# Performance work log

Measured on AMD Instinct MI355X. Metric: run time of the kernel, lower is better.

Reference implementation:

```python
import jax, jax.numpy as jnp
import numpy as np

N_NODES = 50000
N_EDGES = 800000
D = 256          # in_features == out_features == num_classes
T = 4            # number of replicas / linear heads
NS = 64          # num_edges (hyperedges)


def setup_inputs() -> dict:
    key = jax.random.key(0)
    ks = jax.random.split(key, 10)
    s = D ** -0.5
    return {
        "edge_index": jax.random.randint(ks[0], (2, N_EDGES), 0, N_NODES, dtype=jnp.int64)
        if jax.config.jax_enable_x64 else jax.random.randint(ks[0], (2, N_EDGES), 0, N_NODES, dtype=jnp.int32),
        "features": jax.random.normal(ks[1], (N_NODES, D), jnp.float32),
        "lin_w": jax.random.normal(ks[2], (T, D, D), jnp.float32) * s,
        "lin_b": jax.random.normal(ks[3], (T, D), jnp.float32) * 0.01,
        "gcn0_w": jax.random.normal(ks[4], (D, D), jnp.float32) * s,
        "gcn0_b": jax.random.normal(ks[5], (D,), jnp.float32) * 0.01,
        "gcn1_w": jax.random.normal(ks[6], (D, D), jnp.float32) * s,
        "gcn1_b": jax.random.normal(ks[7], (D,), jnp.float32) * 0.01,
        "lin1_w": jax.random.normal(ks[8], (D, NS), jnp.float32) * s,
        "lin1_b": jax.random.normal(ks[9], (NS,), jnp.float32) * 0.01,
    }


def _l2_normalize(x, eps=1e-8):
    n = jnp.sqrt(jnp.sum(x * x, axis=-1, keepdims=True))
    return x / jnp.maximum(n, eps)


def reference(edge_index, features, lin_w, lin_b, gcn0_w, gcn0_b, gcn1_w, gcn1_b, lin1_w, lin1_b):
    num_nodes, d = features.shape
    t = lin_w.shape[0]
    ns = lin1_w.shape[1]
    scale = d ** -0.5  # out_features ** -0.5

    # t linear projections: (t, N, D)
    transformed = jnp.einsum('nd,tdk->tnk', features, lin_w) + lin_b[:, None, :]

    src, dst = edge_index[0], edge_index[1]
    # cosine similarity of features[src] vs each replica's transformed[dst]
    fs = _l2_normalize(features)[src]              # (E, D)
    tf_n = _l2_normalize(transformed)              # (t, N, D)
    sim = jnp.stack([jnp.sum(fs * tf_n[i][dst], axis=-1) for i in range(t)], axis=1)  # (E, t)
    best_idx = jnp.argmax(sim, axis=1)
    best_dst = dst + best_idx.astype(dst.dtype) * num_nodes

    # extra per-replica identity edges: node n -> node n + i*N, i in [0, t)
    ar = jnp.arange(num_nodes, dtype=src.dtype)
    extra_src = jnp.tile(ar, t)
    extra_dst = (ar[None, :] + (jnp.arange(t, dtype=src.dtype) * num_nodes)[:, None]).reshape(-1)

    src_all = jnp.concatenate([src, src, extra_src])
    dst_all = jnp.concatenate([dst, best_dst, extra_dst])
    n_total = (t + 1) * num_nodes

    # PyG gcn_norm: drop pre-existing self loops (weight 0), add one self loop per node,
    # symmetric normalization with degree from destination index.
    loops = jnp.arange(n_total, dtype=src.dtype)
    src2 = jnp.concatenate([src_all, loops])
    dst2 = jnp.concatenate([dst_all, loops])
    w2 = jnp.concatenate([jnp.where(src_all == dst_all, 0.0, 1.0).astype(features.dtype),
                          jnp.ones(n_total, features.dtype)])
    deg = jax.ops.segment_sum(w2, dst2, num_segments=n_total)
    dinv = jnp.where(deg > 0, jax.lax.rsqrt(deg), 0.0)
    norm = w2 * dinv[src2] * dinv[dst2]

    def gcn(x, W, b):
        xw = x @ W
        return jax.ops.segment_sum(norm[:, None] * xw[src2], dst2, num_segments=n_total) + b

    all_features = jnp.concatenate([features, transformed.reshape(t * num_nodes, d)], axis=0)
    # dropout is identity in eval mode
    h = jax.nn.relu(all_features)
    h = gcn(h, gcn0_w, gcn0_b)
    h = jax.nn.relu(h)
    all_features2 = gcn(h, gcn1_w, gcn1_b)          # ((t+1)N, D)
    logits = jax.nn.relu(all_features2) @ lin1_w + lin1_b  # ((t+1)N, NS)

    # H[n, c] counts how many of the (t+1) replicas assign node n to cluster c
    classes = jnp.argmax(logits.reshape(t + 1, num_nodes, ns), axis=-1)  # (t+1, N)
    H = jax.nn.one_hot(classes, ns, dtype=features.dtype).sum(axis=0)     # (N, NS)

    # hyperedge features: sum of all_features2 over base-replica nodes in each hyperedge
    mask = (H > 0).astype(features.dtype)                                  # (N, NS)
    hyperedge_features = mask.T @ all_features2[:num_nodes]                # (NS, D)

    dots = (all_features @ hyperedge_features.T) * scale                   # ((t+1)N, NS)
    return H, hyperedge_features, dots
```

## Files before the change

### kernel.cpp

```cpp
#include <hip/hip_runtime.h>

#define D 256
#define T 4
#define NS 64

typedef unsigned int uint32;
typedef short s16x8 __attribute__((ext_vector_type(8)));
typedef float f32x4 __attribute__((ext_vector_type(4)));

__device__ __forceinline__ float bflo(uint32 u) { return __uint_as_float(u << 16); }
__device__ __forceinline__ float bfhi(uint32 u) { return __uint_as_float(u & 0xffff0000u); }
__device__ __forceinline__ unsigned short f2bf(float x) {
    uint32 u = __float_as_uint(x);
    u = u + 0x7FFFu + ((u >> 16) & 1u);
    return (unsigned short)(u >> 16);
}
__device__ __forceinline__ uint32 pack2(float a, float b) {
    return (uint32)f2bf(a) | ((uint32)f2bf(b) << 16);
}
__device__ __forceinline__ uint32 relu2(uint32 u) {
    uint32 s = u & 0x80008000u;
    uint32 m = ((s >> 15) ^ 0x00010001u) * 0xFFFFu;
    return u & m;
}

__global__ void zero_kernel(uint32* __restrict__ p, long long n)
{
    long long i = (long long)blockIdx.x * blockDim.x + threadIdx.x;
    long long st = (long long)gridDim.x * blockDim.x;
    for (; i < n; i += st) p[i] = 0u;
}

__global__ void f2bf_kernel(const float* __restrict__ in, unsigned short* __restrict__ out,
                            long long n8)
{
    long long i = (long long)blockIdx.x * blockDim.x + threadIdx.x;
    long long st = (long long)gridDim.x * blockDim.x;
    for (; i < n8; i += st) {
        float4 a = *(const float4*)(in + i * 8);
        float4 b = *(const float4*)(in + i * 8 + 4);
        uint4 o;
        o.x = pack2(a.x, a.y); o.y = pack2(a.z, a.w);
        o.z = pack2(b.x, b.y); o.w = pack2(b.z, b.w);
        *(uint4*)(out + i * 8) = o;
    }
}

__global__ void wfrag_kernel(const float* __restrict__ g0, const float* __restrict__ g1,
                             const float* __restrict__ lw, unsigned short* __restrict__ out)
{
    int o = blockIdx.x * 256 + threadIdx.x;
    int mat = blockIdx.y;
    const float* W = (mat == 0) ? g0 : (mat == 1) ? g1 : (lw + (size_t)(mat - 2) * 65536);
    int j = o & 7, lane = (o >> 3) & 63, ks = (o >> 9) & 7, nt = o >> 12;
    int n15 = lane & 15, quad = lane >> 4;
    int k = ks * 32 + quad * 8 + j;
    int n = nt * 16 + n15;
    out[(size_t)mat * 65536 + o] = f2bf(W[(size_t)k * 256 + n]);
}

__global__ __launch_bounds__(256, 2)
void gemm_mfma(const unsigned short* __restrict__ A,
               const unsigned short* __restrict__ Wfrag,
               const float* __restrict__ bias,
               unsigned short* __restrict__ Cout,
               int M, int nStripes)
{
    __shared__ unsigned short Asm[64 * 264];
    int t = threadIdx.x, w = t >> 6, lane = t & 63;
    int n15 = lane & 15, quad = lane >> 4;
    int z = blockIdx.y;
    Wfrag += (size_t)z * 65536;
    bias  += (size_t)z * 256;
    Cout  += (size_t)z * (size_t)M * 256;

    s16x8 bfr[4][8];
#pragma unroll
    for (int nt = 0; nt < 4; nt++)
#pragma unroll
        for (int ks = 0; ks < 8; ks++)
            bfr[nt][ks] = *(const s16x8*)(Wfrag +
                (size_t)(((w * 4 + nt) * 8 + ks) * 64 + lane) * 8);

    float bcol[4];
#pragma unroll
    for (int nt = 0; nt < 4; nt++) bcol[nt] = bias[(w * 4 + nt) * 16 + n15];

    for (int s = blockIdx.x; s < nStripes; s += gridDim.x) {
        int m0 = s * 64;
        __syncthreads();
#pragma unroll
        for (int i = 0; i < 8; i++) {
            int idx = i * 256 + t;
            int m = idx >> 5, kc = (idx & 31) * 8;
            int gm = m0 + m;
            uint4 v = make_uint4(0u, 0u, 0u, 0u);
            if (gm < M) v = *(const uint4*)(A + (size_t)gm * 256 + kc);
            *(uint4*)(Asm + m * 264 + kc) = v;
        }
        __syncthreads();

        f32x4 acc[4][4];
#pragma unroll
        for (int rt = 0; rt < 4; rt++)
#pragma unroll
            for (int nt = 0; nt < 4; nt++)
#pragma unroll
                for (int e = 0; e < 4; e++) acc[rt][nt][e] = 0.f;

#pragma unroll
        for (int rt = 0; rt < 4; rt++) {
            int abase = (rt * 16 + n15) * 264 + quad * 8;
#pragma unroll
            for (int ks = 0; ks < 8; ks++) {
                s16x8 a = *(const s16x8*)(Asm + abase + ks * 32);
#pragma unroll
                for (int nt = 0; nt < 4; nt++)
                    acc[rt][nt] = __builtin_amdgcn_mfma_f32_16x16x32_bf16(
                        a, bfr[nt][ks], acc[rt][nt], 0, 0, 0);
            }
        }

#pragma unroll
        for (int rt = 0; rt < 4; rt++) {
            int row0 = m0 + rt * 16 + quad * 4;
#pragma unroll
            for (int nt = 0; nt < 4; nt++) {
                int colp = (w * 4 + nt) * 16 + n15;
#pragma unroll
                for (int r = 0; r < 4; r++) {
                    int gr = row0 + r;
                    if (gr < M)
                        Cout[(size_t)gr * 256 + colp] = f2bf(acc[rt][nt][r] + bcol[nt]);
                }
            }
        }
    }
}

__global__ __launch_bounds__(256)
void tinv_kernel(const unsigned short* __restrict__ tr, float* __restrict__ tinv, int rows)
{
    int wave = threadIdx.x >> 6, lane = threadIdx.x & 63;
    int r = blockIdx.x * 4 + wave;
    if (r >= rows) return;
    uint2 q = *(const uint2*)(tr + (size_t)r * D + lane * 4);
    float a = bflo(q.x), b = bfhi(q.x), c = bflo(q.y), d = bfhi(q.y);
    float s = a * a + b * b + c * c + d * d;
#pragma unroll
    for (int off = 32; off; off >>= 1) s += __shfl_xor(s, off);
    if (lane == 0) tinv[r] = 1.f / fmaxf(sqrtf(s), 1e-8f);
}

__global__ void ehist_kernel(const int* __restrict__ dst, int* __restrict__ ecnt, int E)
{
    for (int e = blockIdx.x * blockDim.x + threadIdx.x; e < E;
         e += gridDim.x * blockDim.x)
        atomicAdd(ecnt + dst[e], 1);
}

__global__ void escatter_kernel(const int* __restrict__ src, const int* __restrict__ dst,
                                const int* __restrict__ eptr, int* __restrict__ efill,
                                uint2* __restrict__ esorted, int E)
{
    for (int e = blockIdx.x * blockDim.x + threadIdx.x; e < E;
         e += gridDim.x * blockDim.x) {
        int d = dst[e];
        int pos = eptr[d] + atomicAdd(efill + d, 1);
        esorted[pos] = make_uint2((uint32)src[e], (uint32)d);
    }
}

__global__ __launch_bounds__(256)
void sim3_kernel(const uint2* __restrict__ esorted,
                 const unsigned short* __restrict__ featb,
                 const unsigned short* __restrict__ tr, const float* __restrict__ tinv,
                 int* __restrict__ bestS, int E, int Nn)
{
    int w = threadIdx.x >> 6, lane = threadIdx.x & 63;
    int n15 = lane & 15, quad = lane >> 4;
    int base = (blockIdx.x * 4 + w) * 16;
    if (base >= E) return;
    int ei = min(base + n15, E - 1);
    uint2 se = esorted[ei];
    const unsigned short* arow = featb + (size_t)se.x * D + quad * 8;
    const unsigned short* brow = tr + (size_t)se.y * D + quad * 8;
    size_t rstride = (size_t)Nn * D;

    f32x4 a0 = {0.f, 0.f, 0.f, 0.f}, a1 = a0, a2 = a0, a3 = a0;
#pragma unroll
    for (int ks = 0; ks < 8; ks++) {
        s16x8 a  = *(const s16x8*)(arow + ks * 32);
        s16x8 b0 = *(const s16x8*)(brow + ks * 32);
        s16x8 b1 = *(const s16x8*)(brow + rstride + ks * 32);
        s16x8 b2 = *(const s16x8*)(brow + 2 * rstride + ks * 32);
        s16x8 b3 = *(const s16x8*)(brow + 3 * rstride + ks * 32);
        a0 = __builtin_amdgcn_mfma_f32_16x16x32_bf16(a, b0, a0, 0, 0, 0);
        a1 = __builtin_amdgcn_mfma_f32_16x16x32_bf16(a, b1, a1, 0, 0, 0);
        a2 = __builtin_amdgcn_mfma_f32_16x16x32_bf16(a, b2, a2, 0, 0, 0);
        a3 = __builtin_amdgcn_mfma_f32_16x16x32_bf16(a, b3, a3, 0, 0, 0);
    }
    if (quad == (n15 >> 2) && base + n15 < E) {
        int r = n15 & 3;
        int d = (int)se.y;
        float v0 = a0[r] * tinv[d];
        float v1 = a1[r] * tinv[Nn + d];
        float v2 = a2[r] * tinv[2 * Nn + d];
        float v3 = a3[r] * tinv[3 * Nn + d];
        float bv = v0; int bi = 0;
        if (v1 > bv) { bv = v1; bi = 1; }
        if (v2 > bv) { bv = v2; bi = 2; }
        if (v3 > bv) { bv = v3; bi = 3; }
        bestS[base + n15] = bi;
    }
}

__device__ __forceinline__ void decode_edge(int e, const uint2* __restrict__ esorted,
                                            const int* __restrict__ bestS,
                                            int E, int Nn, int& s, int& d, bool& keep)
{
    if (e < E) {
        uint2 se = esorted[e];
        s = (int)se.x; d = (int)se.y; keep = (s != d);
    } else if (e < 2 * E) {
        int k = e - E;
        uint2 se = esorted[k];
        s = (int)se.x; d = (int)se.y + bestS[k] * Nn; keep = (s != d);
    } else if (e < 2 * E + T * Nn) {
        int k = e - 2 * E; int i = k / Nn; int n = k - i * Nn;
        s = n; d = n + i * Nn; keep = (i != 0);
    } else {
        int v = e - (2 * E + T * Nn); s = v; d = v; keep = true;
    }
}

__global__ void hist_kernel(const uint2* __restrict__ esorted, const int* __restrict__ bestS,
                            int* __restrict__ cnt, int E, int Nn)
{
    int total = 2 * E + (2 * T + 1) * Nn;
    for (int e = blockIdx.x * blockDim.x + threadIdx.x; e < total;
         e += gridDim.x * blockDim.x) {
        int s, d; bool keep;
        decode_edge(e, esorted, bestS, E, Nn, s, d, keep);
        if (keep) atomicAdd(cnt + d, 1);
    }
}

__global__ void dinv_kernel(const int* __restrict__ cnt, float* __restrict__ dinv, int n)
{
    int v = blockIdx.x * blockDim.x + threadIdx.x;
    if (v < n) dinv[v] = (cnt[v] > 0) ? rsqrtf((float)cnt[v]) : 0.f;
}

__global__ void emeta_kernel(const uint2* __restrict__ esorted, const int* __restrict__ bestS,
                             const float* __restrict__ dinv, uint2* __restrict__ emeta, int E)
{
    for (int e = blockIdx.x * blockDim.x + threadIdx.x; e < E;
         e += gridDim.x * blockDim.x) {
        uint2 se = esorted[e];
        uint32 packed = se.x | ((uint32)bestS[e] << 27);
        emeta[e] = make_uint2(packed, __float_as_uint(dinv[se.x]));
    }
}

__global__ void scan_sums(const int* __restrict__ cnt, int* __restrict__ aux, int n)
{
    __shared__ int sd[256];
    int idx = blockIdx.x * 256 + threadIdx.x;
    sd[threadIdx.x] = (idx < n) ? cnt[idx] : 0;
    __syncthreads();
    for (int off = 128; off; off >>= 1) {
        if (threadIdx.x < off) sd[threadIdx.x] += sd[threadIdx.x + off];
        __syncthreads();
    }
    if (threadIdx.x == 0) aux[blockIdx.x] = sd[0];
}

__global__ void scan_aux(const int* __restrict__ aux, int* __restrict__ auxex, int nb)
{
    __shared__ int sd[1024];
    int t = threadIdx.x;
    int v = (t < nb) ? aux[t] : 0;
    sd[t] = v;
    __syncthreads();
    for (int off = 1; off < 1024; off <<= 1) {
        int x = (t >= off) ? sd[t - off] : 0;
        __syncthreads();
        sd[t] += x;
        __syncthreads();
    }
    if (t < nb) auxex[t] = sd[t] - v;
}

__global__ void scan_write(const int* __restrict__ cnt, const int* __restrict__ auxex,
                           int* __restrict__ rowptr, int n)
{
    __shared__ int sd[256];
    int t = threadIdx.x;
    int idx = blockIdx.x * 256 + t;
    int v = (idx < n) ? cnt[idx] : 0;
    sd[t] = v;
    __syncthreads();
    for (int off = 1; off < 256; off <<= 1) {
        int x = (t >= off) ? sd[t - off] : 0;
        __syncthreads();
        sd[t] += x;
        __syncthreads();
    }
    if (idx < n) {
        int rp = auxex[blockIdx.x] + sd[t] - v;
        rowptr[idx] = rp;
        if (idx == n - 1) rowptr[n] = rp + v;
    }
}

__global__ __launch_bounds__(256)
void agg5_kernel(const int* __restrict__ eptr, const uint2* __restrict__ emeta,
                 const unsigned short* __restrict__ xa,
                 const unsigned short* __restrict__ xb,
                 const float* __restrict__ dinv,
                 unsigned short* __restrict__ outb, int Nn)
{
    int wave = threadIdx.x >> 6, lane = threadIdx.x & 63;
    int v = blockIdx.x * 4 + wave;
    if (v >= Nn) return;

    float dv  = dinv[v];
    float dr1 = dinv[v + Nn];
    float dr2 = dinv[v + 2 * Nn];
    float dr3 = dinv[v + 3 * Nn];
    float dr4 = dinv[v + 4 * Nn];

    uint2 qv = *(const uint2*)(xa + (size_t)v * D + lane * 4);
    qv.x = relu2(qv.x); qv.y = relu2(qv.y);
    float y0 = bflo(qv.x), y1 = bfhi(qv.x), y2 = bflo(qv.y), y3 = bfhi(qv.y);

    float wsb = dv * dv;
    float b0 = wsb * y0, b1 = wsb * y1, b2 = wsb * y2, b3 = wsb * y3;

    float wi1 = dv * dr1, wi2 = dv * dr2, wi3 = dv * dr3;
    float r10 = wi1 * y0, r11 = wi1 * y1, r12 = wi1 * y2, r13 = wi1 * y3;
    float r20 = wi2 * y0, r21 = wi2 * y1, r22 = wi2 * y2, r23 = wi2 * y3;
    float r30 = wi3 * y0, r31 = wi3 * y1, r32 = wi3 * y2, r33 = wi3 * y3;
    float r40 = 0.f, r41 = 0.f, r42 = 0.f, r43 = 0.f;

    {
        uint2 q = *(const uint2*)(xb + ((size_t)0 * Nn + v) * D + lane * 4);
        q.x = relu2(q.x); q.y = relu2(q.y);
        float ws = dr1 * dr1;
        r10 = fmaf(ws, bflo(q.x), r10); r11 = fmaf(ws, bfhi(q.x), r11);
        r12 = fmaf(ws, bflo(q.y), r12); r13 = fmaf(ws, bfhi(q.y), r13);
    }
    {
        uint2 q = *(const uint2*)(xb + ((size_t)1 * Nn + v) * D + lane * 4);
        q.x = relu2(q.x); q.y = relu2(q.y);
        float ws = dr2 * dr2;
        r20 = fmaf(ws, bflo(q.x), r20); r21 = fmaf(ws, bfhi(q.x), r21);
        r22 = fmaf(ws, bflo(q.y), r22); r23 = fmaf(ws, bfhi(q.y), r23);
    }
    {
        uint2 q = *(const uint2*)(xb + ((size_t)2 * Nn + v) * D + lane * 4);
        q.x = relu2(q.x); q.y = relu2(q.y);
        float ws = dr3 * dr3;
        r30 = fmaf(ws, bflo(q.x), r30); r31 = fmaf(ws, bfhi(q.x), r31);
        r32 = fmaf(ws, bflo(q.y), r32); r33 = fmaf(ws, bfhi(q.y), r33);
    }
    {
        uint2 q = *(const uint2*)(xb + ((size_t)3 * Nn + v) * D + lane * 4);
        q.x = relu2(q.x); q.y = relu2(q.y);
        float ws = dr4 * dr4;
        r40 = fmaf(ws, bflo(q.x), r40); r41 = fmaf(ws, bfhi(q.x), r41);
        r42 = fmaf(ws, bflo(q.y), r42); r43 = fmaf(ws, bfhi(q.y), r43);
    }

    int j = eptr[v], jend = eptr[v + 1];

#define EDGE_BODY(qq, ss, bb, ww)                                                  \
    {                                                                              \
        float x0 = bflo(qq.x), x1 = bfhi(qq.x), x2 = bflo(qq.y), x3 = bfhi(qq.y);  \
        float wb = (ss != v) ? (ww) * dv : 0.f;                                    \
        if (bb == 0) wb += wb;                                                     \
        b0 = fmaf(wb, x0, b0); b1 = fmaf(wb, x1, b1);                              \
        b2 = fmaf(wb, x2, b2); b3 = fmaf(wb, x3, b3);                              \
        if (bb == 1) {                                                             \
            float wr = (ww) * dr1;                                                 \
            r10 = fmaf(wr, x0, r10); r11 = fmaf(wr, x1, r11);                      \
            r12 = fmaf(wr, x2, r12); r13 = fmaf(wr, x3, r13);                      \
        } else if (bb == 2) {                                                      \
            float wr = (ww) * dr2;                                                 \
            r20 = fmaf(wr, x0, r20); r21 = fmaf(wr, x1, r21);                      \
            r22 = fmaf(wr, x2, r22); r23 = fmaf(wr, x3, r23);                      \
        } else if (bb == 3) {                                                      \
            float wr = (ww) * dr3;                                                 \
            r30 = fmaf(wr, x0, r30); r31 = fmaf(wr, x1, r31);                      \
            r32 = fmaf(wr, x2, r32); r33 = fmaf(wr, x3, r33);                      \
        }                                                                          \
    }

    for (; j + 2 <= jend; j += 2) {
        uint2 m0 = emeta[j];
        uint2 m1 = emeta[j + 1];
        uint32 su0 = (uint32)__builtin_amdgcn_readfirstlane((int)m0.x);
        uint32 su1 = (uint32)__builtin_amdgcn_readfirstlane((int)m1.x);
        float ws0 = __uint_as_float((uint32)__builtin_amdgcn_readfirstlane((int)m0.y));
        float ws1 = __uint_as_float((uint32)__builtin_amdgcn_readfirstlane((int)m1.y));
        int s0 = (int)(su0 & 0x07FFFFFFu), bx0 = (int)(su0 >> 27);
        int s1 = (int)(su1 & 0x07FFFFFFu), bx1 = (int)(su1 >> 27);
        uint2 q0 = *(const uint2*)(xa + (size_t)s0 * D + lane * 4);
        uint2 q1 = *(const uint2*)(xa + (size_t)s1 * D + lane * 4);
        q0.x = relu2(q0.x); q0.y = relu2(q0.y);
        q1.x = relu2(q1.x); q1.y = relu2(q1.y);
        EDGE_BODY(q0, s0, bx0, ws0);
        EDGE_BODY(q1, s1, bx1, ws1);
    }
    if (j < jend) {
        uint2 m0 = emeta[j];
        uint32 su0 = (uint32)__builtin_amdgcn_readfirstlane((int)m0.x);
        float ws0 = __uint_as_float((uint32)__builtin_amdgcn_readfirstlane((int)m0.y));
        int s0 = (int)(su0 & 0x07FFFFFFu), bx0 = (int)(su0 >> 27);
        uint2 q0 = *(const uint2*)(xa + (size_t)s0 * D + lane * 4);
        q0.x = relu2(q0.x); q0.y = relu2(q0.y);
        EDGE_BODY(q0, s0, bx0, ws0);
    }
#undef EDGE_BODY

    uint2 o;
    o.x = pack2(b0, b1); o.y = pack2(b2, b3);
    *(uint2*)(outb + (size_t)v * D + lane * 4) = o;
    o.x = pack2(r10, r11); o.y = pack2(r12, r13);
    *(uint2*)(outb + ((size_t)v + Nn) * D + lane * 4) = o;
    o.x = pack2(r20, r21); o.y = pack2(r22, r23);
    *(uint2*)(outb + ((size_t)v + 2 * (size_t)Nn) * D + lane * 4) = o;
    o.x = pack2(r30, r31); o.y = pack2(r32, r33);
    *(uint2*)(outb + ((size_t)v + 3 * (size_t)Nn) * D + lane * 4) = o;
    o.x = pack2(r40, r41); o.y = pack2(r42, r43);
    *(uint2*)(outb + ((size_t)v + 4 * (size_t)Nn) * D + lane * 4) = o;
}

__global__ __launch_bounds__(256, 2)
void logits_mfma(const unsigned short* __restrict__ af2, const float* __restrict__ Wl,
                 const float* __restrict__ bl, float* __restrict__ H,
                 int M, int Nn, int nStripes)
{
    __shared__ unsigned short Asm[64 * 264];
    int t = threadIdx.x, w = t >> 6, lane = t & 63;
    int n15 = lane & 15, quad = lane >> 4;

    s16x8 bfr[4][8];
#pragma unroll
    for (int nt = 0; nt < 4; nt++)
#pragma unroll
        for (int ks = 0; ks < 8; ks++) {
            s16x8 f;
#pragma unroll
            for (int j = 0; j < 8; j++) {
                int k = ks * 32 + quad * 8 + j;
                f[j] = (short)f2bf(Wl[(size_t)k * NS + nt * 16 + n15]);
            }
            bfr[nt][ks] = f;
        }
    float bcol[4];
#pragma unroll
    for (int nt = 0; nt < 4; nt++) bcol[nt] = bl[nt * 16 + n15];

    for (int s = blockIdx.x; s < nStripes; s += gridDim.x) {
        int m0 = s * 64;
        __syncthreads();
#pragma unroll
        for (int i = 0; i < 8; i++) {
            int idx = i * 256 + t;
            int m = idx >> 5, kc = (idx & 31) * 8;
            int gm = m0 + m;
            uint4 v = make_uint4(0u, 0u, 0u, 0u);
            if (gm < M) {
                v = *(const uint4*)(af2 + (size_t)gm * 256 + kc);
                v.x = relu2(v.x); v.y = relu2(v.y);
                v.z = relu2(v.z); v.w = relu2(v.w);
            }
            *(uint4*)(Asm + m * 264 + kc) = v;
        }
        __syncthreads();

        f32x4 acc[4];
#pragma unroll
        for (int nt = 0; nt < 4; nt++)
#pragma unroll
            for (int e = 0; e < 4; e++) acc[nt][e] = 0.f;

        int abase = (w * 16 + n15) * 264 + quad * 8;
#pragma unroll
        for (int ks = 0; ks < 8; ks++) {
            s16x8 a = *(const s16x8*)(Asm + abase + ks * 32);
#pragma unroll
            for (int nt = 0; nt < 4; nt++)
                acc[nt] = __builtin_amdgcn_mfma_f32_16x16x32_bf16(
                    a, bfr[nt][ks], acc[nt], 0, 0, 0);
        }

#pragma unroll
        for (int e = 0; e < 4; e++) {
            float bv = acc[0][e] + bcol[0]; int bi = n15;
#pragma unroll
            for (int nt = 1; nt < 4; nt++) {
                float v = acc[nt][e] + bcol[nt];
                int c = nt * 16 + n15;
                if (v > bv) { bv = v; bi = c; }
            }
#pragma unroll
            for (int off = 1; off < 16; off <<= 1) {
                float ov = __shfl_xor(bv, off);
                int   oi = __shfl_xor(bi, off);
                if (ov > bv || (ov == bv && oi < bi)) { bv = ov; bi = oi; }
            }
            if (n15 == 0) {
                int gr = m0 + w * 16 + quad * 4 + e;
                if (gr < M) atomicAdd(H + (size_t)(gr % Nn) * NS + bi, 1.0f);
            }
        }
    }
}

__global__ __launch_bounds__(256)
void maskTb_kernel(const float* __restrict__ H, unsigned short* __restrict__ maskTb,
                   int Nn, int Kpad)
{
    __shared__ unsigned short tile[64 * 72];
    int t = threadIdx.x;
    int n0 = blockIdx.x * 64;
    int c = t & 63, rr = t >> 6;
#pragma unroll
    for (int i = 0; i < 16; i++) {
        int n = rr + i * 4;
        float hv = (n0 + n < Nn) ? H[(size_t)(n0 + n) * NS + c] : 0.f;
        tile[c * 72 + n] = (hv > 0.f) ? (unsigned short)0x3F80 : (unsigned short)0;
    }
    __syncthreads();
#pragma unroll
    for (int i = 0; i < 4; i++) {
        int idx = i * 256 + t;
        int cc = idx >> 4, ch = idx & 15;
        if (idx < 512) {
            cc = idx >> 3; ch = idx & 7;
            uint4 v = *(const uint4*)(tile + cc * 72 + ch * 8);
            *(uint4*)(maskTb + (size_t)cc * Kpad + n0 + ch * 8) = v;
        }
    }
}

__global__ __launch_bounds__(256, 2)
void he_gemm(const unsigned short* __restrict__ maskTb,
             const unsigned short* __restrict__ af2,
             float* __restrict__ partials, int Kpad)
{
    __shared__ unsigned short Bsm[32 * 264];
    int t = threadIdx.x, w = t >> 6, lane = t & 63;
    int n15 = lane & 15, quad = lane >> 4;
    int k0 = blockIdx.x * 256;

    f32x4 acc[4][4];
#pragma unroll
    for (int mt = 0; mt < 4; mt++)
#pragma unroll
        for (int nt = 0; nt < 4; nt++)
#pragma unroll
            for (int e = 0; e < 4; e++) acc[mt][nt][e] = 0.f;

    for (int s = 0; s < 8; s++) {
        int k = k0 + s * 32;
        __syncthreads();
#pragma unroll
        for (int i = 0; i < 4; i++) {
            int idx = i * 256 + t;
            int row = idx >> 5, col8 = (idx & 31) * 8;
            uint4 v = *(const uint4*)(af2 + (size_t)(k + row) * 256 + col8);
            *(uint4*)(Bsm + row * 264 + col8) = v;
        }
        __syncthreads();

        s16x8 a[4];
#pragma unroll
        for (int mt = 0; mt < 4; mt++)
            a[mt] = *(const s16x8*)(maskTb + (size_t)(mt * 16 + n15) * Kpad
                                    + k + quad * 8);
#pragma unroll
        for (int nt = 0; nt < 4; nt++) {
            int ncol = w * 64 + nt * 16 + n15;
            s16x8 b;
#pragma unroll
            for (int j = 0; j < 8; j++)
                b[j] = (short)Bsm[(quad * 8 + j) * 264 + ncol];
#pragma unroll
            for (int mt = 0; mt < 4; mt++)
                acc[mt][nt] = __builtin_amdgcn_mfma_f32_16x16x32_bf16(
                    a[mt], b, acc[mt][nt], 0, 0, 0);
        }
    }

    float* pdst = partials + (size_t)blockIdx.x * (64 * 256);
#pragma unroll
    for (int mt = 0; mt < 4; mt++)
#pragma unroll
        for (int nt = 0; nt < 4; nt++)
#pragma unroll
            for (int r = 0; r < 4; r++) {
                int m = mt * 16 + quad * 4 + r;
                int n = w * 64 + nt * 16 + n15;
                pdst[(size_t)m * 256 + n] = acc[mt][nt][r];
            }
}

__global__ __launch_bounds__(256)
void he_reduce2(const float* __restrict__ partials, float* __restrict__ he, int KB)
{
    int idx = blockIdx.x * 256 + threadIdx.x;
    float s = 0.f;
    for (int b = 0; b < KB; b++)
        s += partials[(size_t)b * 16384 + idx];
    he[idx] = s;
}

__global__ void bigb_copy(const float* __restrict__ he, float* __restrict__ BigB)
{
    int idx = blockIdx.x * 256 + threadIdx.x;
    if (idx < D * NS) {
        int d = idx >> 6, c = idx & 63;
        BigB[idx] = he[(size_t)c * D + d];
    }
}

__global__ __launch_bounds__(256)
void bigb_mm(const float* __restrict__ lin_w, const float* __restrict__ lin_b,
             const float* __restrict__ he, float* __restrict__ BigB,
             float* __restrict__ beta)
{
    int gw = (int)((blockIdx.x * 256 + threadIdx.x) >> 6);
    int lane = threadIdx.x & 63;
    const int totalA = T * D * NS;
    if (gw >= totalA + T * NS) return;
    const float* xrow; const float* hrow; float* outp;
    if (gw < totalA) {
        int t = gw / (D * NS); int rem = gw - t * D * NS;
        int d = rem / NS; int c = rem - d * NS;
        xrow = lin_w + ((size_t)t * D + d) * D;
        hrow = he + (size_t)c * D;
        outp = BigB + ((size_t)(t + 1) * D + d) * NS + c;
    } else {
        int i = gw - totalA; int t = i / NS; int c = i - t * NS;
        xrow = lin_b + (size_t)t * D;
        hrow = he + (size_t)c * D;
        outp = beta + (size_t)(t + 1) * NS + c;
    }
    float4 x = *(const float4*)(xrow + lane * 4);
    float4 h = *(const float4*)(hrow + lane * 4);
    float s = x.x * h.x + x.y * h.y + x.z * h.z + x.w * h.w;
#pragma unroll
    for (int off = 32; off; off >>= 1) s += __shfl_xor(s, off);
    if (lane == 0) *outp = s;
}

__global__ __launch_bounds__(256, 2)
void dots_mfma(const unsigned short* __restrict__ featb,
               const float* __restrict__ feat32, int useBf,
               const float* __restrict__ BigB,
               const float* __restrict__ beta, float* __restrict__ dots,
               int Nn, int nStripes)
{
    __shared__ unsigned short Asm[64 * 264];
    int t = threadIdx.x, w = t >> 6, lane = t & 63;
    int n15 = lane & 15, quad = lane >> 4;
    int rho = blockIdx.y;
    const float* Bp = BigB + (size_t)rho * D * NS;

    s16x8 bfr[4][8];
#pragma unroll
    for (int nt = 0; nt < 4; nt++)
#pragma unroll
        for (int ks = 0; ks < 8; ks++) {
            s16x8 f;
#pragma unroll
            for (int j = 0; j < 8; j++) {
                int k = ks * 32 + quad * 8 + j;
                f[j] = (short)f2bf(Bp[(size_t)k * NS + nt * 16 + n15]);
            }
            bfr[nt][ks] = f;
        }
    float bcol[4];
#pragma unroll
    for (int nt = 0; nt < 4; nt++) bcol[nt] = beta[rho * NS + nt * 16 + n15];

    for (int s = blockIdx.x; s < nStripes; s += gridDim.x) {
        int m0 = s * 64;
        __syncthreads();
#pragma unroll
        for (int i = 0; i < 8; i++) {
            int idx = i * 256 + t;
            int m = idx >> 5, kc = (idx & 31) * 8;
            int gm = m0 + m;
            uint4 o = make_uint4(0u, 0u, 0u, 0u);
            if (gm < Nn) {
                if (useBf) {
                    o = *(const uint4*)(featb + (size_t)gm * 256 + kc);
                } else {
                    float4 a = *(const float4*)(feat32 + (size_t)gm * 256 + kc);
                    float4 b = *(const float4*)(feat32 + (size_t)gm * 256 + kc + 4);
                    o.x = pack2(a.x, a.y); o.y = pack2(a.z, a.w);
                    o.z = pack2(b.x, b.y); o.w = pack2(b.z, b.w);
                }
            }
            *(uint4*)(Asm + m * 264 + kc) = o;
        }
        __syncthreads();

        f32x4 acc[4];
#pragma unroll
        for (int nt = 0; nt < 4; nt++)
#pragma unroll
            for (int e = 0; e < 4; e++) acc[nt][e] = 0.f;

        int abase = (w * 16 + n15) * 264 + quad * 8;
#pragma unroll
        for (int ks = 0; ks < 8; ks++) {
            s16x8 a = *(const s16x8*)(Asm + abase + ks * 32);
#pragma unroll
            for (int nt = 0; nt < 4; nt++)
                acc[nt] = __builtin_amdgcn_mfma_f32_16x16x32_bf16(
                    a, bfr[nt][ks], acc[nt], 0, 0, 0);
        }

#pragma unroll
        for (int e = 0; e < 4; e++) {
            int gr = m0 + w * 16 + quad * 4 + e;
            if (gr >= Nn) continue;
#pragma unroll
            for (int nt = 0; nt < 4; nt++) {
                int c = nt * 16 + n15;
                dots[((size_t)rho * Nn + gr) * NS + c] = (acc[nt][e] + bcol[nt]) * 0.0625f;
            }
        }
    }
}

extern "C" void kernel_launch(void* const* d_in, const int* in_sizes, int n_in,
                              void* d_out, int out_size, void* d_ws, size_t ws_size,
                              hipStream_t stream)
{
    const int*   edge_index = (const int*)d_in[0];
    const float* features   = (const float*)d_in[1];
    const float* lin_w      = (const float*)d_in[2];
    const float* lin_b      = (const float*)d_in[3];
    const float* gcn0_w     = (const float*)d_in[4];
    const float* gcn0_b     = (const float*)d_in[5];
    const float* gcn1_w     = (const float*)d_in[6];
    const float* gcn1_b     = (const float*)d_in[7];
    const float* lin1_w     = (const float*)d_in[8];
    const float* lin1_b     = (const float*)d_in[9];

    int E  = in_sizes[0] / 2;
    int Nn = in_sizes[1] / D;
    int n_total = (T + 1) * Nn;
    int Mrep = T * Nn;

    const int* src = edge_index;
    const int* dst = edge_index + E;

    float* out_H    = (float*)d_out;
    float* out_he   = out_H + (size_t)Nn * NS;
    float* out_dots = out_he + (size_t)NS * D;

    int KB   = (Nn + 255) / 256;
    int Kpad = KB * 256;

    char* ws0 = (char*)d_ws;
    char* wsp = ws0;
    auto carve = [&](size_t bytes) {
        char* p = wsp; wsp += (bytes + 255) & ~(size_t)255; return p;
    };
    unsigned short* R1   = (unsigned short*)carve((size_t)n_total * D * 2);
    unsigned short* R2   = (unsigned short*)carve((size_t)n_total * D * 2);
    float*          BigB = (float*)carve((size_t)(T + 1) * D * NS * 4);
    float*          beta = (float*)carve((size_t)(T + 1) * NS * 4);
    unsigned short* transformed = R2;

    size_t featb_bytes = (size_t)Nn * D * 2;
    unsigned short* featb = nullptr;
    int useBfDots = 0;
    if ((size_t)(wsp - ws0) + featb_bytes + 256 <= ws_size) {
        featb = (unsigned short*)carve(featb_bytes);
        useBfDots = 1;
    }

    char* sc = (char*)out_dots;
    auto carve2 = [&](size_t bytes) {
        char* p = sc; sc += (bytes + 255) & ~(size_t)255; return p;
    };
    float* tinv    = (float*)carve2((size_t)Mrep * 4);
    int*   best    = (int*)carve2((size_t)E * 4);
    int*   cnt     = (int*)carve2((size_t)n_total * 4);
    float* dinv    = (float*)carve2((size_t)n_total * 4);
    int*   aux     = (int*)carve2(1024 * 4);
    int*   auxex   = (int*)carve2(1024 * 4);
    if (!featb) featb = (unsigned short*)carve2(featb_bytes);
    unsigned short* Wfrags = (unsigned short*)carve2((size_t)6 * 65536 * 2);
    int*   ecnt    = (int*)carve2((size_t)Nn * 4);
    int*   eptr    = (int*)carve2((size_t)(Nn + 1) * 4);
    int*   efill   = (int*)carve2((size_t)Nn * 4);
    uint2* esorted = (uint2*)carve2((size_t)E * 8);
    uint2* emeta   = (uint2*)carve2((size_t)E * 8);
    unsigned short* maskTb = (unsigned short*)carve2((size_t)NS * Kpad * 2);

    float* partials = (float*)R1;

    zero_kernel<<<512, 256, 0, stream>>>((uint32*)cnt, n_total);
    zero_kernel<<<512, 256, 0, stream>>>((uint32*)ecnt, Nn);
    zero_kernel<<<512, 256, 0, stream>>>((uint32*)efill, Nn);
    zero_kernel<<<512, 256, 0, stream>>>((uint32*)out_H, (long long)Nn * NS + NS * D);
    zero_kernel<<<1, 256, 0, stream>>>((uint32*)beta, (T + 1) * NS);

    wfrag_kernel<<<dim3(256, 6), 256, 0, stream>>>(gcn0_w, gcn1_w, lin_w, Wfrags);
    f2bf_kernel<<<2048, 256, 0, stream>>>(features, featb, (long long)Nn * D / 8);

    int strN = (Nn + 63) / 64;
    gemm_mfma<<<dim3(512, T), 256, 0, stream>>>(featb, Wfrags + 2 * 65536, lin_b,
                                                transformed, Nn, strN);
    tinv_kernel<<<(Mrep + 3) / 4, 256, 0, stream>>>(transformed, tinv, Mrep);

    ehist_kernel<<<2048, 256, 0, stream>>>(dst, ecnt, E);
    int enb = (Nn + 255) / 256;
    scan_sums<<<enb, 256, 0, stream>>>(ecnt, aux, Nn);
    scan_aux<<<1, 1024, 0, stream>>>(aux, auxex, enb);
    scan_write<<<enb, 256, 0, stream>>>(ecnt, auxex, eptr, Nn);
    escatter_kernel<<<2048, 256, 0, stream>>>(src, dst, eptr, efill, esorted, E);
    int nGroups = (E + 15) / 16;
    sim3_kernel<<<(nGroups + 3) / 4, 256, 0, stream>>>(esorted, featb, transformed,
                                                       tinv, best, E, Nn);

    hist_kernel<<<2048, 256, 0, stream>>>(esorted, best, cnt, E, Nn);
    dinv_kernel<<<(n_total + 255) / 256, 256, 0, stream>>>(cnt, dinv, n_total);
    emeta_kernel<<<2048, 256, 0, stream>>>(esorted, best, dinv, emeta, E);

    int strT = (n_total + 63) / 64;
    agg5_kernel<<<(Nn + 3) / 4, 256, 0, stream>>>(eptr, emeta, featb, transformed,
                                                  dinv, R1, Nn);
    gemm_mfma<<<dim3(512, 1), 256, 0, stream>>>(R1, Wfrags, gcn0_b, R1, n_total, strT);

    agg5_kernel<<<(Nn + 3) / 4, 256, 0, stream>>>(eptr, emeta, R1, R1 + (size_t)Nn * D,
                                                  dinv, R2, Nn);
    gemm_mfma<<<dim3(512, 1), 256, 0, stream>>>(R2, Wfrags + 65536, gcn1_b, R2,
                                                n_total, strT);

    logits_mfma<<<512, 256, 0, stream>>>(R2, lin1_w, lin1_b, out_H, n_total, Nn, strT);

    maskTb_kernel<<<Kpad / 64, 256, 0, stream>>>(out_H, maskTb, Nn, Kpad);
    he_gemm<<<KB, 256, 0, stream>>>(maskTb, R2, partials, Kpad);
    he_reduce2<<<64, 256, 0, stream>>>(partials, out_he, KB);

    bigb_copy<<<(D * NS + 255) / 256, 256, 0, stream>>>(out_he, BigB);
    bigb_mm<<<(T * D * NS + T * NS + 3) / 4, 256, 0, stream>>>(lin_w, lin_b, out_he,
                                                               BigB, beta);
    dots_mfma<<<dim3(160, 5), 256, 0, stream>>>(featb, features, useBfDots,
                                                BigB, beta, out_dots, Nn, strN);
}
```

Before: 1.005 ms.

## Interleave replica outputs per node so similarity gathers read contiguous rows

The transformed projections are now stored node-major with the four replica rows adjacent (row = node*4 + replica), rather than replica-major. The edge-similarity kernel then reads all four replica rows for a destination node from one contiguous 2KB region, and it loads the source feature fragments once into registers before four separate MFMA passes. The GEMM and aggregation kernels gain stride parameters to write and read this layout, and the mask transpose loop drops a dead branch. The tinv indexing changes to match. The aim is better cache-line and locality use for the random gathers, at the cost of more registers held for the preloaded A fragments.

```diff
diff --git a/kernel.cpp b/kernel.cpp
--- a/kernel.cpp
+++ b/kernel.cpp
@@ -64,7 +64,7 @@
                const unsigned short* __restrict__ Wfrag,
                const float* __restrict__ bias,
                unsigned short* __restrict__ Cout,
-               int M, int nStripes)
+               int M, int nStripes, int rowMul, int zRowAdd)
 {
     __shared__ unsigned short Asm[64 * 264];
     int t = threadIdx.x, w = t >> 6, lane = t & 63;
@@ -72,7 +72,6 @@
     int z = blockIdx.y;
     Wfrag += (size_t)z * 65536;
     bias  += (size_t)z * 256;
-    Cout  += (size_t)z * (size_t)M * 256;
 
     s16x8 bfr[4][8];
 #pragma unroll
@@ -130,8 +129,10 @@
 #pragma unroll
                 for (int r = 0; r < 4; r++) {
                     int gr = row0 + r;
-                    if (gr < M)
-                        Cout[(size_t)gr * 256 + colp] = f2bf(acc[rt][nt][r] + bcol[nt]);
+                    if (gr < M) {
+                        size_t ro = (size_t)gr * rowMul + (size_t)z * zRowAdd;
+                        Cout[ro * 256 + colp] = f2bf(acc[rt][nt][r] + bcol[nt]);
+                    }
                 }
             }
         }
@@ -172,9 +173,9 @@
 }
 
 __global__ __launch_bounds__(256)
-void sim3_kernel(const uint2* __restrict__ esorted,
+void sim4_kernel(const uint2* __restrict__ esorted,
                  const unsigned short* __restrict__ featb,
-                 const unsigned short* __restrict__ tr, const float* __restrict__ tinv,
+                 const unsigned short* __restrict__ trI, const float* __restrict__ tinv,
                  int* __restrict__ bestS, int E, int Nn)
 {
     int w = threadIdx.x >> 6, lane = threadIdx.x & 63;
@@ -184,29 +185,41 @@
     int ei = min(base + n15, E - 1);
     uint2 se = esorted[ei];
     const unsigned short* arow = featb + (size_t)se.x * D + quad * 8;
-    const unsigned short* brow = tr + (size_t)se.y * D + quad * 8;
-    size_t rstride = (size_t)Nn * D;
+    const unsigned short* brow = trI + ((size_t)se.y * 4) * D + quad * 8;
+
+    s16x8 a[8];
+#pragma unroll
+    for (int ks = 0; ks < 8; ks++) a[ks] = *(const s16x8*)(arow + ks * 32);
 
     f32x4 a0 = {0.f, 0.f, 0.f, 0.f}, a1 = a0, a2 = a0, a3 = a0;
 #pragma unroll
     for (int ks = 0; ks < 8; ks++) {
-        s16x8 a  = *(const s16x8*)(arow + ks * 32);
         s16x8 b0 = *(const s16x8*)(brow + ks * 32);
-        s16x8 b1 = *(const s16x8*)(brow + rstride + ks * 32);
-        s16x8 b2 = *(const s16x8*)(brow + 2 * rstride + ks * 32);
-        s16x8 b3 = *(const s16x8*)(brow + 3 * rstride + ks * 32);
-        a0 = __builtin_amdgcn_mfma_f32_16x16x32_bf16(a, b0, a0, 0, 0, 0);
-        a1 = __builtin_amdgcn_mfma_f32_16x16x32_bf16(a, b1, a1, 0, 0, 0);
-        a2 = __builtin_amdgcn_mfma_f32_16x16x32_bf16(a, b2, a2, 0, 0, 0);
-        a3 = __builtin_amdgcn_mfma_f32_16x16x32_bf16(a, b3, a3, 0, 0, 0);
-    }
+        a0 = __builtin_amdgcn_mfma_f32_16x16x32_bf16(a[ks], b0, a0, 0, 0, 0);
+    }
+#pragma unroll
+    for (int ks = 0; ks < 8; ks++) {
+        s16x8 b1 = *(const s16x8*)(brow + D + ks * 32);
+        a1 = __builtin_amdgcn_mfma_f32_16x16x32_bf16(a[ks], b1, a1, 0, 0, 0);
+    }
+#pragma unroll
+    for (int ks = 0; ks < 8; ks++) {
+        s16x8 b2 = *(const s16x8*)(brow + 2 * D + ks * 32);
+        a2 = __builtin_amdgcn_mfma_f32_16x16x32_bf16(a[ks], b2, a2, 0, 0, 0);
+    }
+#pragma unroll
+    for (int ks = 0; ks < 8; ks++) {
+        s16x8 b3 = *(const s16x8*)(brow + 3 * D + ks * 32);
+        a3 = __builtin_amdgcn_mfma_f32_16x16x32_bf16(a[ks], b3, a3, 0, 0, 0);
+    }
+
     if (quad == (n15 >> 2) && base + n15 < E) {
         int r = n15 & 3;
-        int d = (int)se.y;
-        float v0 = a0[r] * tinv[d];
-        float v1 = a1[r] * tinv[Nn + d];
-        float v2 = a2[r] * tinv[2 * Nn + d];
-        float v3 = a3[r] * tinv[3 * Nn + d];
+        int d4 = (int)se.y * 4;
+        float v0 = a0[r] * tinv[d4];
+        float v1 = a1[r] * tinv[d4 + 1];
+        float v2 = a2[r] * tinv[d4 + 2];
+        float v3 = a3[r] * tinv[d4 + 3];
         float bv = v0; int bi = 0;
         if (v1 > bv) { bv = v1; bi = 1; }
         if (v2 > bv) { bv = v2; bi = 2; }
@@ -319,7 +332,7 @@
                  const unsigned short* __restrict__ xa,
                  const unsigned short* __restrict__ xb,
                  const float* __restrict__ dinv,
-                 unsigned short* __restrict__ outb, int Nn)
+                 unsigned short* __restrict__ outb, int Nn, int xrm, int xra)
 {
     int wave = threadIdx.x >> 6, lane = threadIdx.x & 63;
     int v = blockIdx.x * 4 + wave;
@@ -345,28 +358,28 @@
     float r40 = 0.f, r41 = 0.f, r42 = 0.f, r43 = 0.f;
 
     {
-        uint2 q = *(const uint2*)(xb + ((size_t)0 * Nn + v) * D + lane * 4);
+        uint2 q = *(const uint2*)(xb + ((size_t)v * xrm + 0 * (size_t)xra) * D + lane * 4);
         q.x = relu2(q.x); q.y = relu2(q.y);
         float ws = dr1 * dr1;
         r10 = fmaf(ws, bflo(q.x), r10); r11 = fmaf(ws, bfhi(q.x), r11);
         r12 = fmaf(ws, bflo(q.y), r12); r13 = fmaf(ws, bfhi(q.y), r13);
     }
     {
-        uint2 q = *(const uint2*)(xb + ((size_t)1 * Nn + v) * D + lane * 4);
+        uint2 q = *(const uint2*)(xb + ((size_t)v * xrm + 1 * (size_t)xra) * D + lane * 4);
         q.x = relu2(q.x); q.y = relu2(q.y);
         float ws = dr2 * dr2;
         r20 = fmaf(ws, bflo(q.x), r20); r21 = fmaf(ws, bfhi(q.x), r21);
         r22 = fmaf(ws, bflo(q.y), r22); r23 = fmaf(ws, bfhi(q.y), r23);
     }
     {
-        uint2 q = *(const uint2*)(xb + ((size_t)2 * Nn + v) * D + lane * 4);
+        uint2 q = *(const uint2*)(xb + ((size_t)v * xrm + 2 * (size_t)xra) * D + lane * 4);
         q.x = relu2(q.x); q.y = relu2(q.y);
         float ws = dr3 * dr3;
         r30 = fmaf(ws, bflo(q.x), r30); r31 = fmaf(ws, bfhi(q.x), r31);
         r32 = fmaf(ws, bflo(q.y), r32); r33 = fmaf(ws, bfhi(q.y), r33);
     }
     {
-        uint2 q = *(const uint2*)(xb + ((size_t)3 * Nn + v) * D + lane * 4);
+        uint2 q = *(const uint2*)(xb + ((size_t)v * xrm + 3 * (size_t)xra) * D + lane * 4);
         q.x = relu2(q.x); q.y = relu2(q.y);
         float ws = dr4 * dr4;
         r40 = fmaf(ws, bflo(q.x), r40); r41 = fmaf(ws, bfhi(q.x), r41);
@@ -536,14 +549,11 @@
     }
     __syncthreads();
 #pragma unroll
-    for (int i = 0; i < 4; i++) {
+    for (int i = 0; i < 2; i++) {
         int idx = i * 256 + t;
-        int cc = idx >> 4, ch = idx & 15;
-        if (idx < 512) {
-            cc = idx >> 3; ch = idx & 7;
-            uint4 v = *(const uint4*)(tile + cc * 72 + ch * 8);
-            *(uint4*)(maskTb + (size_t)cc * Kpad + n0 + ch * 8) = v;
-        }
+        int cc = idx >> 3, ch = idx & 7;
+        uint4 v = *(const uint4*)(tile + cc * 72 + ch * 8);
+        *(uint4*)(maskTb + (size_t)cc * Kpad + n0 + ch * 8) = v;
     }
 }
 
@@ -779,7 +789,7 @@
     unsigned short* R2   = (unsigned short*)carve((size_t)n_total * D * 2);
     float*          BigB = (float*)carve((size_t)(T + 1) * D * NS * 4);
     float*          beta = (float*)carve((size_t)(T + 1) * NS * 4);
-    unsigned short* transformed = R2;
+    unsigned short* trI  = R2;
 
     size_t featb_bytes = (size_t)Nn * D * 2;
     unsigned short* featb = nullptr;
@@ -821,8 +831,8 @@
 
     int strN = (Nn + 63) / 64;
     gemm_mfma<<<dim3(512, T), 256, 0, stream>>>(featb, Wfrags + 2 * 65536, lin_b,
-                                                transformed, Nn, strN);
-    tinv_kernel<<<(Mrep + 3) / 4, 256, 0, stream>>>(transformed, tinv, Mrep);
+                                                trI, Nn, strN, T, 1);
+    tinv_kernel<<<(Mrep + 3) / 4, 256, 0, stream>>>(trI, tinv, Mrep);
 
     ehist_kernel<<<2048, 256, 0, stream>>>(dst, ecnt, E);
     int enb = (Nn + 255) / 256;
@@ -831,7 +841,7 @@
     scan_write<<<enb, 256, 0, stream>>>(ecnt, auxex, eptr, Nn);
     escatter_kernel<<<2048, 256, 0, stream>>>(src, dst, eptr, efill, esorted, E);
     int nGroups = (E + 15) / 16;
-    sim3_kernel<<<(nGroups + 3) / 4, 256, 0, stream>>>(esorted, featb, transformed,
+    sim4_kernel<<<(nGroups + 3) / 4, 256, 0, stream>>>(esorted, featb, trI,
                                                        tinv, best, E, Nn);
 
     hist_kernel<<<2048, 256, 0, stream>>>(esorted, best, cnt, E, Nn);
@@ -839,14 +849,15 @@
     emeta_kernel<<<2048, 256, 0, stream>>>(esorted, best, dinv, emeta, E);
 
     int strT = (n_total + 63) / 64;
-    agg5_kernel<<<(Nn + 3) / 4, 256, 0, stream>>>(eptr, emeta, featb, transformed,
-                                                  dinv, R1, Nn);
-    gemm_mfma<<<dim3(512, 1), 256, 0, stream>>>(R1, Wfrags, gcn0_b, R1, n_total, strT);
+    agg5_kernel<<<(Nn + 3) / 4, 256, 0, stream>>>(eptr, emeta, featb, trI,
+                                                  dinv, R1, Nn, 4, 1);
+    gemm_mfma<<<dim3(512, 1), 256, 0, stream>>>(R1, Wfrags, gcn0_b, R1, n_total,
+                                                strT, 1, 0);
 
     agg5_kernel<<<(Nn + 3) / 4, 256, 0, stream>>>(eptr, emeta, R1, R1 + (size_t)Nn * D,
-                                                  dinv, R2, Nn);
+                                                  dinv, R2, Nn, 1, Nn);
     gemm_mfma<<<dim3(512, 1), 256, 0, stream>>>(R2, Wfrags + 65536, gcn1_b, R2,
-                                                n_total, strT);
+                                                n_total, strT, 1, 0);
 
     logits_mfma<<<512, 256, 0, stream>>>(R2, lin1_w, lin1_b, out_H, n_total, Nn, strT);
 
```

Result: no change. 1.016 ms (+1.1%).
